# Kernel tuning notes

Measured on AMD Instinct MI355X. Metric: run time of the kernel, lower is better.

The kernel has to match this reference:

```python
import jax, jax.numpy as jnp
import numpy as np

K = 3

def setup_inputs() -> dict:
    key = jax.random.key(0)
    k1, k2, k3, k4 = jax.random.split(key, 4)
    B, N, F_in, T, F_out = 8, 2048, 16, 12, 32
    x = jax.random.normal(k1, (B, N, F_in, T), dtype=jnp.float32)
    spatial_attention = jax.random.uniform(k2, (B, N, N), dtype=jnp.float32)
    node_embeddings = jax.random.normal(k3, (N, 16), dtype=jnp.float32)
    theta = jax.random.normal(k4, (K, F_in, F_out), dtype=jnp.float32) * 0.1
    return {"x": x, "spatial_attention": spatial_attention,
            "node_embeddings": node_embeddings, "theta": theta}

def _cheb_polys(node_embeddings, N, K):
    # supports = softmax(relu(E E^T), axis=1)
    supports = jax.nn.softmax(jax.nn.relu(node_embeddings @ node_embeddings.T), axis=1)
    polys = [jnp.eye(N, dtype=supports.dtype), supports]
    for _ in range(2, K):
        polys.append(2.0 * supports @ polys[-1] - polys[-2])
    return jnp.stack(polys[:K], axis=0)  # (K, N, N)

def reference(x, spatial_attention, node_embeddings, theta):
    B, N, F_in, T = x.shape
    polys = _cheb_polys(node_embeddings, N, K)             # (K,N,N)
    # T_k_with_at = polys[k] * attention (broadcast over batch);
    # rhs = T_k_with_at^T @ graph_signal for every timestep:
    # (K,N,N)*(B,N,N) contracted with (B,N,F,T) over source node n -> (K,B,M,F,T)
    rhs = jnp.einsum('knm,bnm,bnft->kbmft', polys, spatial_attention, x)
    # accumulate rhs @ theta_k over k -> (B,M,F_out,T)
    out = jnp.einsum('kbmft,kfo->bmot', rhs, theta)
    return jax.nn.relu(out)
```

## Files before the change

kernel.cpp:

```cpp
#include <hip/hip_runtime.h>

#define NN    2048
#define BATCH 8
#define FIN   16
#define TT    12
#define FOUT  32
#define FT    (FIN*TT)
#define OT    (FOUT*TT)

typedef unsigned short ushort_t;
typedef __attribute__((ext_vector_type(8))) short   short8;
typedef __attribute__((ext_vector_type(4))) float   f32x4;
typedef __attribute__((ext_vector_type(4))) unsigned short us4;
typedef __attribute__((ext_vector_type(8))) unsigned short us8;

__device__ __forceinline__ float b2f(unsigned short u) {
    union { unsigned int i; float f; } v; v.i = ((unsigned int)u) << 16; return v.f;
}
__device__ __forceinline__ unsigned short f2b(float f) {
    union { float f; unsigned int i; } v; v.f = f;
    unsigned int x = v.i;
    x += 0x7fffu + ((x >> 16) & 1u);
    return (unsigned short)(x >> 16);
}

__global__ __launch_bounds__(256)
void k_supports(const float* __restrict__ E, ushort_t* __restrict__ Sb) {
    const int n = blockIdx.x;
    __shared__ float row[NN];
    __shared__ float red[256];
    const int tid = threadIdx.x;

    float en[16];
    #pragma unroll
    for (int j = 0; j < 16; ++j) en[j] = E[n * 16 + j];

    float lmax = 0.0f;
    for (int m = tid; m < NN; m += 256) {
        float d = 0.0f;
        #pragma unroll
        for (int j = 0; j < 16; ++j) d += en[j] * E[m * 16 + j];
        d = fmaxf(d, 0.0f);
        row[m] = d;
        lmax = fmaxf(lmax, d);
    }
    red[tid] = lmax; __syncthreads();
    for (int s = 128; s > 0; s >>= 1) {
        if (tid < s) red[tid] = fmaxf(red[tid], red[tid + s]);
        __syncthreads();
    }
    const float mx = red[0];
    __syncthreads();

    float lsum = 0.0f;
    for (int m = tid; m < NN; m += 256) {
        float e = __expf(row[m] - mx);
        row[m] = e;
        lsum += e;
    }
    red[tid] = lsum; __syncthreads();
    for (int s = 128; s > 0; s >>= 1) {
        if (tid < s) red[tid] += red[tid + s];
        __syncthreads();
    }
    const float inv = 1.0f / red[0];
    for (int m = tid; m < NN; m += 256) Sb[(size_t)n * NN + m] = f2b(row[m] * inv);
}

__global__ __launch_bounds__(256)
void k_pack_st(const ushort_t* __restrict__ Sb, ushort_t* __restrict__ SbT) {
    const int r0 = blockIdx.x * 64, c0 = blockIdx.y * 64;
    __shared__ ushort_t Lt[64][65];
    const int tid = threadIdx.x;
    #pragma unroll
    for (int p = 0; p < 2; ++p) {
        const int i = (tid >> 3) + p * 32;
        const int j8 = (tid & 7) * 8;
        us8 v = *(const us8*)&Sb[(size_t)(r0 + i) * NN + c0 + j8];
        #pragma unroll
        for (int e = 0; e < 8; ++e) Lt[i][j8 + e] = v[e];
    }
    __syncthreads();
    #pragma unroll
    for (int p = 0; p < 2; ++p) {
        const int jj = (tid >> 3) + p * 32;
        const int i8 = (tid & 7) * 8;
        us8 v;
        #pragma unroll
        for (int e = 0; e < 8; ++e) v[e] = Lt[i8 + e][jj];
        *(us8*)&SbT[(size_t)(c0 + jj) * NN + r0 + i8] = v;
    }
}

__global__ __launch_bounds__(256)
void k_pack_x(const float* __restrict__ x, ushort_t* __restrict__ xbT) {
    const int nc = blockIdx.x * 64;
    const int b  = blockIdx.y;
    __shared__ ushort_t Lt[FT][65];
    const int tid = threadIdx.x;
    const float* __restrict__ xb = x + (size_t)b * NN * FT;
    #pragma unroll
    for (int p = 0; p < 12; ++p) {
        const int id = tid + 256 * p;
        const int nn = id / 48;
        const int f4 = (id % 48) * 4;
        const float4 v = *(const float4*)&xb[(size_t)(nc + nn) * FT + f4];
        Lt[f4 + 0][nn] = f2b(v.x);
        Lt[f4 + 1][nn] = f2b(v.y);
        Lt[f4 + 2][nn] = f2b(v.z);
        Lt[f4 + 3][nn] = f2b(v.w);
    }
    __syncthreads();
    #pragma unroll
    for (int p = 0; p < 6; ++p) {
        const int id = tid + 256 * p;
        const int ft = id >> 3;
        const int n8 = (id & 7) * 8;
        us8 v;
        #pragma unroll
        for (int e = 0; e < 8; ++e) v[e] = Lt[ft][n8 + e];
        *(us8*)&xbT[((size_t)b * FT + ft) * NN + nc + n8] = v;
    }
}

__global__ __launch_bounds__(256)
void k_t2(const ushort_t* __restrict__ Sb, const ushort_t* __restrict__ SbT,
          ushort_t* __restrict__ T2b) {
    const int m0 = blockIdx.x * 64;
    const int n0 = blockIdx.y * 128;
    __shared__ __align__(16) ushort_t As[128 * 64];
    __shared__ __align__(16) ushort_t Bs[64 * 64];
    const int tid = threadIdx.x;
    const int lane = tid & 63, w = tid >> 6;
    const int l15 = lane & 15, q = lane >> 4, l7 = lane & 7, l3 = lane >> 3;
    const int n0w = (w & 1) * 64, c0w = (w >> 1) * 32;

    f32x4 acc[4][2];
    #pragma unroll
    for (int i = 0; i < 4; ++i)
        #pragma unroll
        for (int j = 0; j < 2; ++j) acc[i][j] = {0.f, 0.f, 0.f, 0.f};

    for (int l0 = 0; l0 < NN; l0 += 64) {
        us8 av[4], bv[2];
        #pragma unroll
        for (int p = 0; p < 4; ++p) {
            const int row = w * 32 + p * 8 + l3;
            av[p] = *(const us8*)&Sb[(size_t)(n0 + row) * NN + l0 + l7 * 8];
        }
        #pragma unroll
        for (int p = 0; p < 2; ++p) {
            const int row = w * 16 + p * 8 + l3;
            bv[p] = *(const us8*)&SbT[(size_t)(m0 + row) * NN + l0 + l7 * 8];
        }
        __syncthreads();
        #pragma unroll
        for (int p = 0; p < 4; ++p) {
            const int row = w * 32 + p * 8 + l3;
            *(us8*)&As[row * 64 + (l7 ^ l3) * 8] = av[p];
        }
        #pragma unroll
        for (int p = 0; p < 2; ++p) {
            const int row = w * 16 + p * 8 + l3;
            *(us8*)&Bs[row * 64 + (l7 ^ l3) * 8] = bv[p];
        }
        __syncthreads();
        #pragma unroll
        for (int s = 0; s < 2; ++s) {
            short8 a[4], bb[2];
            const int u = (s * 4 + q) ^ l7;
            #pragma unroll
            for (int i = 0; i < 4; ++i) {
                const int row = n0w + i * 16 + l15;
                a[i] = *(const short8*)&As[row * 64 + u * 8];
            }
            #pragma unroll
            for (int j = 0; j < 2; ++j) {
                const int col = c0w + j * 16 + l15;
                bb[j] = *(const short8*)&Bs[col * 64 + u * 8];
            }
            #pragma unroll
            for (int i = 0; i < 4; ++i)
                #pragma unroll
                for (int j = 0; j < 2; ++j)
                    acc[i][j] = __builtin_amdgcn_mfma_f32_16x16x32_bf16(a[i], bb[j], acc[i][j], 0, 0, 0);
        }
    }
    #pragma unroll
    for (int i = 0; i < 4; ++i)
        #pragma unroll
        for (int j = 0; j < 2; ++j)
            #pragma unroll
            for (int r = 0; r < 4; ++r) {
                const int ng = n0 + n0w + i * 16 + q * 4 + r;
                const int mg = m0 + c0w + j * 16 + l15;
                const float v = 2.0f * acc[i][j][r] - (ng == mg ? 1.0f : 0.0f);
                T2b[(size_t)ng * NN + mg] = f2b(v);
            }
}

__global__ __launch_bounds__(256)
void k_rhs(const ushort_t* __restrict__ Sb, const ushort_t* __restrict__ T2b,
           const float* __restrict__ att, const ushort_t* __restrict__ xbT,
           float* __restrict__ rhs) {
    const int m0 = blockIdx.x * 32;
    const int b  = blockIdx.y;
    __shared__ __align__(16) ushort_t As[2 * 32 * 72];
    __shared__ __align__(16) ushort_t Xs[FT * 64];
    const int tid = threadIdx.x;
    const int lane = tid & 63, w = tid >> 6;
    const int l15 = lane & 15, q = lane >> 4, l7 = lane & 7, l3 = lane >> 3;
    const int k1 = w & 1, ft0 = (w >> 1) * 96;
    const float* __restrict__ attb = att + (size_t)b * NN * NN;

    const int k1s = tid >> 7;
    const int uu  = tid & 127;
    const int m4  = (uu & 7) * 4;
    const int nn4 = (uu >> 3) * 4;
    const ushort_t* __restrict__ Pk = k1s ? T2b : Sb;

    f32x4 acc[2][6];
    #pragma unroll
    for (int i = 0; i < 2; ++i)
        #pragma unroll
        for (int t = 0; t < 6; ++t) acc[i][t] = {0.f, 0.f, 0.f, 0.f};

    for (int nc = 0; nc < NN; nc += 64) {
        us8 xv[6];
        #pragma unroll
        for (int p = 0; p < 6; ++p) {
            const int row = (w * 6 + p) * 8 + l3;
            xv[p] = *(const us8*)&xbT[((size_t)b * FT + row) * NN + nc + l7 * 8];
        }
        ushort_t Wv[4][4];
        #pragma unroll
        for (int r = 0; r < 4; ++r) {
            const int nn = nc + nn4 + r;
            const us4    pv = *(const us4*)&Pk[(size_t)nn * NN + m0 + m4];
            const float4 av = *(const float4*)&attb[(size_t)nn * NN + m0 + m4];
            Wv[r][0] = f2b(b2f(pv.x) * av.x);
            Wv[r][1] = f2b(b2f(pv.y) * av.y);
            Wv[r][2] = f2b(b2f(pv.z) * av.z);
            Wv[r][3] = f2b(b2f(pv.w) * av.w);
        }
        __syncthreads();
        #pragma unroll
        for (int p = 0; p < 6; ++p) {
            const int row = (w * 6 + p) * 8 + l3;
            *(us8*)&Xs[row * 64 + (l7 ^ l3) * 8] = xv[p];
        }
        #pragma unroll
        for (int c = 0; c < 4; ++c) {
            us4 wv = {Wv[0][c], Wv[1][c], Wv[2][c], Wv[3][c]};
            *(us4*)&As[(k1s * 32 + m4 + c) * 72 + nn4] = wv;
        }
        __syncthreads();
        #pragma unroll
        for (int s = 0; s < 2; ++s) {
            short8 a[2], bb[6];
            #pragma unroll
            for (int i = 0; i < 2; ++i) {
                const int row = i * 16 + l15;
                a[i] = *(const short8*)&As[(k1 * 32 + row) * 72 + s * 32 + q * 8];
            }
            #pragma unroll
            for (int t = 0; t < 6; ++t) {
                const int col = ft0 + t * 16 + l15;
                const int u = (s * 4 + q) ^ (col & 7);
                bb[t] = *(const short8*)&Xs[col * 64 + u * 8];
            }
            #pragma unroll
            for (int i = 0; i < 2; ++i)
                #pragma unroll
                for (int t = 0; t < 6; ++t)
                    acc[i][t] = __builtin_amdgcn_mfma_f32_16x16x32_bf16(a[i], bb[t], acc[i][t], 0, 0, 0);
        }
    }
    float* __restrict__ op = rhs + ((size_t)(k1 * BATCH + b)) * NN * FT;
    #pragma unroll
    for (int i = 0; i < 2; ++i)
        #pragma unroll
        for (int t = 0; t < 6; ++t)
            #pragma unroll
            for (int r = 0; r < 4; ++r) {
                const int mg = m0 + i * 16 + q * 4 + r;
                const int ftg = ft0 + t * 16 + l15;
                op[(size_t)mg * FT + ftg] = acc[i][t][r];
            }
}

__global__ __launch_bounds__(128)
void k_out(const float* __restrict__ x, const float* __restrict__ att,
           const float* __restrict__ theta, const float* __restrict__ rhs,
           float* __restrict__ out) {
    const int m = blockIdx.x & (NN - 1);
    const int b = blockIdx.x >> 11;
    __shared__ float xr[FT], r1[FT], r2[FT];
    __shared__ float th[3 * FIN * FOUT];
    const int tid = threadIdx.x;

    const float* __restrict__ xb = x + ((size_t)b * NN + m) * FT;
    const float* __restrict__ p1 = rhs + ((size_t)0 * BATCH + b) * NN * FT + (size_t)m * FT;
    const float* __restrict__ p2 = rhs + ((size_t)1 * BATCH + b) * NN * FT + (size_t)m * FT;
    const float a0 = att[((size_t)b * NN + m) * NN + m];

    for (int i = tid; i < FT; i += 128) {
        xr[i] = xb[i] * a0;
        r1[i] = p1[i];
        r2[i] = p2[i];
    }
    for (int i = tid; i < 3 * FIN * FOUT; i += 128) th[i] = theta[i];
    __syncthreads();

    float* __restrict__ ob = out + ((size_t)b * NN + m) * OT;
    for (int idx = tid; idx < OT; idx += 128) {
        const int o = idx / TT, t = idx % TT;
        float acc = 0.0f;
        #pragma unroll
        for (int f = 0; f < FIN; ++f) {
            const int ft = f * TT + t;
            acc += th[f * FOUT + o] * xr[ft];
            acc += th[512 + f * FOUT + o] * r1[ft];
            acc += th[1024 + f * FOUT + o] * r2[ft];
        }
        ob[idx] = fmaxf(acc, 0.0f);
    }
}

extern "C" void kernel_launch(void* const* d_in, const int* in_sizes, int n_in,
                              void* d_out, int out_size, void* d_ws, size_t ws_size,
                              hipStream_t stream) {
    const float* x     = (const float*)d_in[0];
    const float* att   = (const float*)d_in[1];
    const float* E     = (const float*)d_in[2];
    const float* theta = (const float*)d_in[3];
    float* out = (float*)d_out;

    ushort_t* Sb  = (ushort_t*)d_ws;
    ushort_t* SbT = Sb  + (size_t)NN * NN;
    ushort_t* T2b = SbT + (size_t)NN * NN;
    ushort_t* xbT = T2b + (size_t)NN * NN;
    float*    rhs = (float*)(xbT + (size_t)BATCH * FT * NN);

    k_supports<<<NN, 256, 0, stream>>>(E, Sb);
    k_pack_st<<<dim3(32, 32), 256, 0, stream>>>(Sb, SbT);
    k_pack_x<<<dim3(32, BATCH), 256, 0, stream>>>(x, xbT);
    k_t2<<<dim3(32, 16), 256, 0, stream>>>(Sb, SbT, T2b);
    k_rhs<<<dim3(64, BATCH), 256, 0, stream>>>(Sb, T2b, att, xbT, rhs);
    k_out<<<BATCH * NN, 128, 0, stream>>>(x, att, theta, rhs, out);
}
```

Before: 352.7 us.

## Double-buffer LDS in T2 and RHS GEMMs with register prefetch, shrink T2 tile

Both the T2 (S@S) GEMM and the attention-weighted RHS GEMM now use ping-pong shared-memory buffers. The next K-slice is loaded from global into registers while MFMAs run on the current buffer, which leaves one barrier per iteration instead of two. The T2 tile shrinks from 128x64 to 64x64 and the grid doubles to raise block count. The RHS A-tile drops the padded 72 stride in favour of an XOR swizzle to avoid bank conflicts. The cost is higher LDS and register use, which may reduce occupancy.

After: 335.2 us. 1.05x faster.

```diff
diff --git a/kernel.cpp b/kernel.cpp
--- a/kernel.cpp
+++ b/kernel.cpp
@@ -127,73 +127,83 @@
 void k_t2(const ushort_t* __restrict__ Sb, const ushort_t* __restrict__ SbT,
           ushort_t* __restrict__ T2b) {
     const int m0 = blockIdx.x * 64;
-    const int n0 = blockIdx.y * 128;
-    __shared__ __align__(16) ushort_t As[128 * 64];
-    __shared__ __align__(16) ushort_t Bs[64 * 64];
+    const int n0 = blockIdx.y * 64;
+    __shared__ __align__(16) ushort_t As[2][64 * 64];
+    __shared__ __align__(16) ushort_t Bs[2][64 * 64];
     const int tid = threadIdx.x;
     const int lane = tid & 63, w = tid >> 6;
-    const int l15 = lane & 15, q = lane >> 4, l7 = lane & 7, l3 = lane >> 3;
-    const int n0w = (w & 1) * 64, c0w = (w >> 1) * 32;
-
-    f32x4 acc[4][2];
-    #pragma unroll
-    for (int i = 0; i < 4; ++i)
+    const int l15 = lane & 15, q = lane >> 4, l7 = lane & 7;
+    const int n0w = (w & 1) * 32, m0w = (w >> 1) * 32;
+    const int sr = tid >> 3;
+    const int sc = tid & 7;
+
+    f32x4 acc[2][2];
+    #pragma unroll
+    for (int i = 0; i < 2; ++i)
         #pragma unroll
         for (int j = 0; j < 2; ++j) acc[i][j] = {0.f, 0.f, 0.f, 0.f};
 
-    for (int l0 = 0; l0 < NN; l0 += 64) {
-        us8 av[4], bv[2];
-        #pragma unroll
-        for (int p = 0; p < 4; ++p) {
-            const int row = w * 32 + p * 8 + l3;
-            av[p] = *(const us8*)&Sb[(size_t)(n0 + row) * NN + l0 + l7 * 8];
-        }
-        #pragma unroll
-        for (int p = 0; p < 2; ++p) {
-            const int row = w * 16 + p * 8 + l3;
-            bv[p] = *(const us8*)&SbT[(size_t)(m0 + row) * NN + l0 + l7 * 8];
-        }
+    us8 av[2], bv[2];
+    #pragma unroll
+    for (int p = 0; p < 2; ++p) {
+        const int row = sr + 32 * p;
+        av[p] = *(const us8*)&Sb[(size_t)(n0 + row) * NN + sc * 8];
+        bv[p] = *(const us8*)&SbT[(size_t)(m0 + row) * NN + sc * 8];
+    }
+    #pragma unroll
+    for (int p = 0; p < 2; ++p) {
+        const int row = sr + 32 * p;
+        const int cs = (sc ^ (row & 7)) * 8;
+        *(us8*)&As[0][row * 64 + cs] = av[p];
+        *(us8*)&Bs[0][row * 64 + cs] = bv[p];
+    }
+    for (int it = 0; it < 32; ++it) {
         __syncthreads();
-        #pragma unroll
-        for (int p = 0; p < 4; ++p) {
-            const int row = w * 32 + p * 8 + l3;
-            *(us8*)&As[row * 64 + (l7 ^ l3) * 8] = av[p];
-        }
-        #pragma unroll
-        for (int p = 0; p < 2; ++p) {
-            const int row = w * 16 + p * 8 + l3;
-            *(us8*)&Bs[row * 64 + (l7 ^ l3) * 8] = bv[p];
-        }
-        __syncthreads();
+        const int cur = it & 1;
+        if (it < 31) {
+            const int l0 = (it + 1) * 64;
+            #pragma unroll
+            for (int p = 0; p < 2; ++p) {
+                const int row = sr + 32 * p;
+                av[p] = *(const us8*)&Sb[(size_t)(n0 + row) * NN + l0 + sc * 8];
+                bv[p] = *(const us8*)&SbT[(size_t)(m0 + row) * NN + l0 + sc * 8];
+            }
+        }
         #pragma unroll
         for (int s = 0; s < 2; ++s) {
-            short8 a[4], bb[2];
-            const int u = (s * 4 + q) ^ l7;
-            #pragma unroll
-            for (int i = 0; i < 4; ++i) {
-                const int row = n0w + i * 16 + l15;
-                a[i] = *(const short8*)&As[row * 64 + u * 8];
-            }
-            #pragma unroll
-            for (int j = 0; j < 2; ++j) {
-                const int col = c0w + j * 16 + l15;
-                bb[j] = *(const short8*)&Bs[col * 64 + u * 8];
-            }
-            #pragma unroll
-            for (int i = 0; i < 4; ++i)
+            short8 a[2], bb[2];
+            const int u = ((s * 4 + q) ^ l7) * 8;
+            #pragma unroll
+            for (int i = 0; i < 2; ++i)
+                a[i] = *(const short8*)&As[cur][(n0w + i * 16 + l15) * 64 + u];
+            #pragma unroll
+            for (int j = 0; j < 2; ++j)
+                bb[j] = *(const short8*)&Bs[cur][(m0w + j * 16 + l15) * 64 + u];
+            #pragma unroll
+            for (int i = 0; i < 2; ++i)
                 #pragma unroll
                 for (int j = 0; j < 2; ++j)
                     acc[i][j] = __builtin_amdgcn_mfma_f32_16x16x32_bf16(a[i], bb[j], acc[i][j], 0, 0, 0);
         }
-    }
-    #pragma unroll
-    for (int i = 0; i < 4; ++i)
+        if (it < 31) {
+            const int nxt = cur ^ 1;
+            #pragma unroll
+            for (int p = 0; p < 2; ++p) {
+                const int row = sr + 32 * p;
+                const int cs = (sc ^ (row & 7)) * 8;
+                *(us8*)&As[nxt][row * 64 + cs] = av[p];
+                *(us8*)&Bs[nxt][row * 64 + cs] = bv[p];
+            }
+        }
+    }
+    #pragma unroll
+    for (int i = 0; i < 2; ++i)
         #pragma unroll
         for (int j = 0; j < 2; ++j)
             #pragma unroll
             for (int r = 0; r < 4; ++r) {
                 const int ng = n0 + n0w + i * 16 + q * 4 + r;
-                const int mg = m0 + c0w + j * 16 + l15;
+                const int mg = m0 + m0w + j * 16 + l15;
                 const float v = 2.0f * acc[i][j][r] - (ng == mg ? 1.0f : 0.0f);
                 T2b[(size_t)ng * NN + mg] = f2b(v);
             }
@@ -205,8 +215,8 @@
            float* __restrict__ rhs) {
     const int m0 = blockIdx.x * 32;
     const int b  = blockIdx.y;
-    __shared__ __align__(16) ushort_t As[2 * 32 * 72];
-    __shared__ __align__(16) ushort_t Xs[FT * 64];
+    __shared__ __align__(16) ushort_t As[2][2 * 32 * 64];
+    __shared__ __align__(16) ushort_t Xs[2][FT * 64];
     const int tid = threadIdx.x;
     const int lane = tid & 63, w = tid >> 6;
     const int l15 = lane & 15, q = lane >> 4, l7 = lane & 7, l3 = lane >> 3;
@@ -225,55 +235,89 @@
         #pragma unroll
         for (int t = 0; t < 6; ++t) acc[i][t] = {0.f, 0.f, 0.f, 0.f};
 
-    for (int nc = 0; nc < NN; nc += 64) {
-        us8 xv[6];
-        #pragma unroll
-        for (int p = 0; p < 6; ++p) {
-            const int row = (w * 6 + p) * 8 + l3;
-            xv[p] = *(const us8*)&xbT[((size_t)b * FT + row) * NN + nc + l7 * 8];
-        }
-        ushort_t Wv[4][4];
-        #pragma unroll
-        for (int r = 0; r < 4; ++r) {
-            const int nn = nc + nn4 + r;
-            const us4    pv = *(const us4*)&Pk[(size_t)nn * NN + m0 + m4];
-            const float4 av = *(const float4*)&attb[(size_t)nn * NN + m0 + m4];
-            Wv[r][0] = f2b(b2f(pv.x) * av.x);
-            Wv[r][1] = f2b(b2f(pv.y) * av.y);
-            Wv[r][2] = f2b(b2f(pv.z) * av.z);
-            Wv[r][3] = f2b(b2f(pv.w) * av.w);
-        }
+    us8   xv[6];
+    us4   pv[4];
+    f32x4 av4[4];
+
+    #pragma unroll
+    for (int p = 0; p < 6; ++p) {
+        const int row = (w * 6 + p) * 8 + l3;
+        xv[p] = *(const us8*)&xbT[((size_t)b * FT + row) * NN + l7 * 8];
+    }
+    #pragma unroll
+    for (int r = 0; r < 4; ++r) {
+        const int nn = nn4 + r;
+        pv[r]  = *(const us4*)&Pk[(size_t)nn * NN + m0 + m4];
+        av4[r] = *(const f32x4*)&attb[(size_t)nn * NN + m0 + m4];
+    }
+    #pragma unroll
+    for (int p = 0; p < 6; ++p) {
+        const int row = (w * 6 + p) * 8 + l3;
+        *(us8*)&Xs[0][row * 64 + (l7 ^ l3) * 8] = xv[p];
+    }
+    #pragma unroll
+    for (int c = 0; c < 4; ++c) {
+        us4 wv;
+        #pragma unroll
+        for (int r = 0; r < 4; ++r) wv[r] = f2b(b2f(pv[r][c]) * av4[r][c]);
+        const int rowm = m4 + c;
+        const int off = (((nn4 >> 3) ^ (rowm & 7)) * 8) + (nn4 & 4);
+        *(us4*)&As[0][(k1s * 32 + rowm) * 64 + off] = wv;
+    }
+
+    for (int it = 0; it < 32; ++it) {
         __syncthreads();
-        #pragma unroll
-        for (int p = 0; p < 6; ++p) {
-            const int row = (w * 6 + p) * 8 + l3;
-            *(us8*)&Xs[row * 64 + (l7 ^ l3) * 8] = xv[p];
-        }
-        #pragma unroll
-        for (int c = 0; c < 4; ++c) {
-            us4 wv = {Wv[0][c], Wv[1][c], Wv[2][c], Wv[3][c]};
-            *(us4*)&As[(k1s * 32 + m4 + c) * 72 + nn4] = wv;
-        }
-        __syncthreads();
+        const int cur = it & 1;
+        if (it < 31) {
+            const int nc = (it + 1) * 64;
+            #pragma unroll
+            for (int p = 0; p < 6; ++p) {
+                const int row = (w * 6 + p) * 8 + l3;
+                xv[p] = *(const us8*)&xbT[((size_t)b * FT + row) * NN + nc + l7 * 8];
+            }
+            #pragma unroll
+            for (int r = 0; r < 4; ++r) {
+                const int nn = nc + nn4 + r;
+                pv[r]  = *(const us4*)&Pk[(size_t)nn * NN + m0 + m4];
+                av4[r] = *(const f32x4*)&attb[(size_t)nn * NN + m0 + m4];
+            }
+        }
         #pragma unroll
         for (int s = 0; s < 2; ++s) {
             short8 a[2], bb[6];
             #pragma unroll
             for (int i = 0; i < 2; ++i) {
                 const int row = i * 16 + l15;
-                a[i] = *(const short8*)&As[(k1 * 32 + row) * 72 + s * 32 + q * 8];
+                a[i] = *(const short8*)&As[cur][(k1 * 32 + row) * 64 + (((s * 4 + q) ^ l7) * 8)];
             }
             #pragma unroll
             for (int t = 0; t < 6; ++t) {
                 const int col = ft0 + t * 16 + l15;
-                const int u = (s * 4 + q) ^ (col & 7);
-                bb[t] = *(const short8*)&Xs[col * 64 + u * 8];
+                const int u = ((s * 4 + q) ^ (col & 7)) * 8;
+                bb[t] = *(const short8*)&Xs[cur][col * 64 + u];
             }
             #pragma unroll
             for (int i = 0; i < 2; ++i)
                 #pragma unroll
                 for (int t = 0; t < 6; ++t)
                     acc[i][t] = __builtin_amdgcn_mfma_f32_16x16x32_bf16(a[i], bb[t], acc[i][t], 0, 0, 0);
+        }
+        if (it < 31) {
+            const int nxt = cur ^ 1;
+            #pragma unroll
+            for (int p = 0; p < 6; ++p) {
+                const int row = (w * 6 + p) * 8 + l3;
+                *(us8*)&Xs[nxt][row * 64 + (l7 ^ l3) * 8] = xv[p];
+            }
+            #pragma unroll
+            for (int c = 0; c < 4; ++c) {
+                us4 wv;
+                #pragma unroll
+                for (int r = 0; r < 4; ++r) wv[r] = f2b(b2f(pv[r][c]) * av4[r][c]);
+                const int rowm = m4 + c;
+                const int off = (((nn4 >> 3) ^ (rowm & 7)) * 8) + (nn4 & 4);
+                *(us4*)&As[nxt][(k1s * 32 + rowm) * 64 + off] = wv;
+            }
         }
     }
     float* __restrict__ op = rhs + ((size_t)(k1 * BATCH + b)) * NN * FT;
@@ -345,7 +389,7 @@
     k_supports<<<NN, 256, 0, stream>>>(E, Sb);
     k_pack_st<<<dim3(32, 32), 256, 0, stream>>>(Sb, SbT);
     k_pack_x<<<dim3(32, BATCH), 256, 0, stream>>>(x, xbT);
-    k_t2<<<dim3(32, 16), 256, 0, stream>>>(Sb, SbT, T2b);
+    k_t2<<<dim3(32, 32), 256, 0, stream>>>(Sb, SbT, T2b);
     k_rhs<<<dim3(64, BATCH), 256, 0, stream>>>(Sb, T2b, att, xbT, rhs);
     k_out<<<BATCH * NN, 128, 0, stream>>>(x, att, theta, rhs, out);
 }
```
